# Optimization experiments

Hardware: AMD Instinct MI355X
Metric: run time of the kernel (lower is better)

## Reference

```python
import jax, jax.numpy as jnp
import numpy as np

# ---- config ----
N = 500000
C = 32            # output_coordinate_dim
RES = [256, 256, 256, 64]
J = 2             # wavelet levels
BOUNDS = 1.3
# plane i -> (H, W) of stored plane, and (q, r) coord indices into [x,y,z,t]
# grid_sample convention: coord0 indexes W, coord1 indexes H
PLANE_RES = [(256, 256), (256, 256), (256, 64), (256, 256), (256, 64), (256, 64)]
COORD_IDX = [(0, 1), (0, 2), (3, 0), (1, 2), (3, 1), (3, 2)]

# coif4 decomposition low-pass filter (pywt), 24 taps
DEC_LO = np.array([
    -1.7849850030882614e-06, -3.2596802368833675e-06, 3.1229875865345646e-05,
    6.233903446100713e-05, -0.00025997455248771324, -0.0005890207562443383,
    0.0012665619292989445, 0.003751436157278457, -0.00565828668661072,
    -0.015211731527946259, 0.025082261844864097, 0.03933442712333749,
    -0.09622044203398798, -0.06662747426342504, 0.4343860564914685,
    0.782238930920499, 0.41530840703043026, -0.05607731331675481,
    -0.08126669968087875, 0.026682300156053072, 0.016068943964776348,
    -0.0073461663276420935, -0.0016294920126017326, 0.0008923136685823146],
    dtype=np.float32)
REC_LO = DEC_LO[::-1].copy()                                    # synthesis low-pass
REC_HI = (DEC_LO * ((-1.0) ** np.arange(DEC_LO.shape[0]))).astype(np.float32)  # QMF high-pass


def _up2(x, axis):
    """Insert zeros between samples along axis (upsample by 2)."""
    x = jnp.moveaxis(x, axis, -1)
    z = jnp.zeros(x.shape[:-1] + (2 * x.shape[-1],), x.dtype)
    z = z.at[..., ::2].set(x)
    return jnp.moveaxis(z, -1, axis)


def _circ_conv(x, f, axis):
    """Circular convolution along axis with a short fixed filter (periodization mode)."""
    out = f[0] * x
    for k in range(1, len(f)):
        out = out + f[k] * jnp.roll(x, k, axis=axis)
    return out


def _sfb1d(lo, hi, axis):
    """1D synthesis filter bank: upsample, filter, add. Length L -> 2L."""
    return _circ_conv(_up2(lo, axis), REC_LO, axis) + _circ_conv(_up2(hi, axis), REC_HI, axis)


def _sfb_level(ll, yh):
    """One inverse-DWT level. ll: [1,C,h,w], yh: [1,C,3,h,w] -> [1,C,2h,2w]."""
    lh, hl, hh = yh[:, :, 0], yh[:, :, 1], yh[:, :, 2]
    lo = _sfb1d(ll, lh, axis=2)   # combine along H
    hi = _sfb1d(hl, hh, axis=2)
    return _sfb1d(lo, hi, axis=3)  # combine along W


def _idwt2(yl, yhb, yha):
    """2-level inverse DWT (coif4, periodization). yl coarsest, yhb coarse detail, yha fine detail."""
    x = _sfb_level(yl, yhb)   # H/4 -> H/2
    x = _sfb_level(x, yha)    # H/2 -> H
    return x                  # [1, C, H, W]


def _bilinear_sample(plane, coords):
    """torch.grid_sample(bilinear, align_corners=True) equivalent.
    plane: [C,H,W]; coords: [N,2] in [-1,1], coords[:,0]->W, coords[:,1]->H. Returns [N,C]."""
    Cc, H, W = plane.shape
    x = jnp.clip((coords[:, 0] + 1.0) * 0.5 * (W - 1), 0.0, W - 1.0)
    y = jnp.clip((coords[:, 1] + 1.0) * 0.5 * (H - 1), 0.0, H - 1.0)
    x0 = jnp.clip(jnp.floor(x), 0.0, W - 2.0)
    y0 = jnp.clip(jnp.floor(y), 0.0, H - 2.0)
    wx = x - x0
    wy = y - y0
    x0i = x0.astype(jnp.int32); x1i = x0i + 1
    y0i = y0.astype(jnp.int32); y1i = y0i + 1
    v = (plane[:, y0i, x0i] * (1 - wy) * (1 - wx)
         + plane[:, y0i, x1i] * (1 - wy) * wx
         + plane[:, y1i, x0i] * wy * (1 - wx)
         + plane[:, y1i, x1i] * wy * wx)  # [C,N]
    return v.T


def setup_inputs() -> dict:
    key = jax.random.key(0)
    keys = jax.random.split(key, 2 + 6 * 3)
    inp = {}
    inp["pts"] = jax.random.uniform(keys[0], (N, 3), jnp.float32, -BOUNDS, BOUNDS)
    inp["timestamps"] = jax.random.uniform(keys[1], (N, 1), jnp.float32, 0.0, 1.0)
    for i, (H, W) in enumerate(PLANE_RES):
        k0, k1, k2 = keys[2 + 3 * i], keys[2 + 3 * i + 1], keys[2 + 3 * i + 2]
        # wavelet-domain learned parameters: yl coarsest approx, yha fine detail, yhb coarse detail
        inp[f"yl{i}"] = 0.3 + 0.1 * jax.random.normal(k0, (1, C, H // 4, W // 4), jnp.float32)
        inp[f"yha{i}"] = 0.05 * jax.random.normal(k1, (1, C, 3, H // 2, W // 2), jnp.float32)
        inp[f"yhb{i}"] = 0.05 * jax.random.normal(k2, (1, C, 3, H // 4, W // 4), jnp.float32)
    return inp


def reference(pts, timestamps,
              yl0, yha0, yhb0, yl1, yha1, yhb1, yl2, yha2, yhb2,
              yl3, yha3, yhb3, yl4, yha4, yhb4, yl5, yha5, yhb5):
    coefs = [(yl0, yha0, yhb0), (yl1, yha1, yhb1), (yl2, yha2, yhb2),
             (yl3, yha3, yhb3), (yl4, yha4, yhb4), (yl5, yha5, yhb5)]
    # normalize_aabb with aabb = [[B,B,B],[-B,-B,-B]]
    pts_n = (pts - BOUNDS) * (2.0 / (-2.0 * BOUNDS)) - 1.0
    t = timestamps * 2.0 - 1.0
    p4 = jnp.concatenate([pts_n, t], axis=-1)  # [N,4] = (x,y,z,t) in [-1,1]
    interp = jnp.ones((), jnp.float32)
    for (yl, yha, yhb), (q, r) in zip(coefs, COORD_IDX):
        plane = _idwt2(yl, yhb, yha)[0]                      # [C,H,W] IDWT reconstruction
        coords = jnp.stack([p4[:, q], p4[:, r]], axis=-1)    # [N,2]
        feat = _bilinear_sample(plane, coords)               # [N,C] gather
        interp = interp * feat                               # multiplicative fusion
    return interp
```

## Files before the change

kernel.cpp:

```cpp
#include <hip/hip_runtime.h>
#include <hip/hip_fp16.h>

#define NBIN 4096
#define CAP 256
#define OVCAP 65536
#define NSB 32

__device__ __constant__ float DEC_LO[24] = {
    -1.7849850030882614e-06f, -3.2596802368833675e-06f, 3.1229875865345646e-05f,
    6.233903446100713e-05f, -0.00025997455248771324f, -0.0005890207562443383f,
    0.0012665619292989445f, 0.003751436157278457f, -0.00565828668661072f,
    -0.015211731527946259f, 0.025082261844864097f, 0.03933442712333749f,
    -0.09622044203398798f, -0.06662747426342504f, 0.4343860564914685f,
    0.782238930920499f, 0.41530840703043026f, -0.05607731331675481f,
    -0.08126669968087875f, 0.026682300156053072f, 0.016068943964776348f,
    -0.0073461663276420935f, -0.0016294920126017326f, 0.0008923136685823146f
};

struct PK {
    const float* yl[6];
    const float* yhb[6];
    const float* yha[6];
    float* x1[6];
    __half* lo2[6];
    __half* hi2[6];
    __half* planeH[6];
    const float* pts;
    const float* ts;
    int* cnt;
    float4* binP4;
    int* binIdx;
    float4* ovP4;
    int* ovIdx;
    int Npts;
};

__device__ __forceinline__ void compute_p4(const float* pts, const float* ts, int p, float* p4) {
    const float sc = (float)(2.0 / (-2.0 * 1.3));
    p4[0] = (pts[p * 3 + 0] - 1.3f) * sc - 1.0f;
    p4[1] = (pts[p * 3 + 1] - 1.3f) * sc - 1.0f;
    p4[2] = (pts[p * 3 + 2] - 1.3f) * sc - 1.0f;
    p4[3] = ts[p] * 2.0f - 1.0f;
}

__device__ __forceinline__ int morton_key(const float* p4) {
    int key = 0;
#pragma unroll
    for (int d = 0; d < 4; ++d) {
        float u = (p4[d] + 1.0f) * 0.5f * 8.0f;
        int ci = (int)u;
        ci = ci < 0 ? 0 : (ci > 7 ? 7 : ci);
#pragma unroll
        for (int b = 0; b < 3; ++b) key |= ((ci >> b) & 1) << (b * 4 + d);
    }
    return key;
}

__global__ __launch_bounds__(256) void k1_l1_zero(PK a) {
    __shared__ struct { float lo[32 * 64], hi[32 * 64]; } sm;
    int bid = blockIdx.x, tid = threadIdx.x;

    if (bid < 768) {
        int rg = bid & 3, c = (bid >> 2) & 31, i = bid >> 7;
        int w4 = (i == 0 || i == 1 || i == 3) ? 64 : 16;
        int lw4 = (w4 == 64) ? 6 : 4;

        const float* llc = a.yl[i] + (size_t)c * 64 * w4;
        const float* lhc = a.yhb[i] + (size_t)(c * 3 + 0) * 64 * w4;
        const float* hlc = a.yhb[i] + (size_t)(c * 3 + 1) * 64 * w4;
        const float* hhc = a.yhb[i] + (size_t)(c * 3 + 2) * 64 * w4;

        for (int idx = tid; idx < (16 << lw4); idx += 256) {
            int mp = idx >> lw4, x = idx & (w4 - 1);
            int m = rg * 16 + mp;
            float lo0 = 0.f, lo1 = 0.f, hi0 = 0.f, hi1 = 0.f;
#pragma unroll
            for (int j = 0; j < 12; ++j) {
                int r = (m - j) & 63;
                int ii = (r << lw4) + x;
                float vll = llc[ii], vlh = lhc[ii], vhl = hlc[ii], vhh = hhc[ii];
                float rl0 = DEC_LO[23 - 2 * j], rl1 = DEC_LO[22 - 2 * j];
                float rh0 = DEC_LO[2 * j],      rh1 = -DEC_LO[2 * j + 1];
                lo0 += rl0 * vll + rh0 * vlh;
                lo1 += rl1 * vll + rh1 * vlh;
                hi0 += rl0 * vhl + rh0 * vhh;
                hi1 += rl1 * vhl + rh1 * vhh;
            }
            sm.lo[((2 * mp) << lw4) + x] = lo0;
            sm.lo[((2 * mp + 1) << lw4) + x] = lo1;
            sm.hi[((2 * mp) << lw4) + x] = hi0;
            sm.hi[((2 * mp + 1) << lw4) + x] = hi1;
        }
        __syncthreads();

        int w2 = w4 * 2;
        float* x1p = a.x1[i] + (size_t)c * 128 * w2;
        for (int idx = tid; idx < (32 << lw4); idx += 256) {
            int yl = idx >> lw4, mcol = idx & (w4 - 1);
            float o0 = 0.f, o1 = 0.f;
#pragma unroll
            for (int j = 0; j < 12; ++j) {
                int r = (mcol - j) & (w4 - 1);
                float vl = sm.lo[(yl << lw4) + r], vh = sm.hi[(yl << lw4) + r];
                o0 += DEC_LO[23 - 2 * j] * vl + DEC_LO[2 * j] * vh;
                o1 += DEC_LO[22 - 2 * j] * vl - DEC_LO[2 * j + 1] * vh;
            }
            *(float2*)(x1p + (size_t)(rg * 32 + yl) * w2 + 2 * mcol) = make_float2(o0, o1);
        }
    } else {
        int idx = (bid - 768) * 256 + tid;
        if (idx <= NBIN) a.cnt[idx] = 0;
    }
}

__global__ __launch_bounds__(256) void k2_v2_scatter(PK a) {
    __shared__ int hist[NBIN];
    int bid = blockIdx.x, tid = threadIdx.x;

    if (bid < NSB) {
        for (int b = tid; b < NBIN; b += 256) hist[b] = 0;
        __syncthreads();

        int chunk = (a.Npts + NSB - 1) / NSB;
        int p0 = bid * chunk;
        int p1 = p0 + chunk; if (p1 > a.Npts) p1 = a.Npts;

        for (int p = p0 + tid; p < p1; p += 256) {
            float p4[4];
            compute_p4(a.pts, a.ts, p, p4);
            atomicAdd(&hist[morton_key(p4)], 1);
        }
        __syncthreads();

        for (int b = tid; b < NBIN; b += 256) {
            int h = hist[b];
            if (h > 0) hist[b] = atomicAdd(&a.cnt[b], h);
        }
        __syncthreads();

        for (int p = p0 + tid; p < p1; p += 256) {
            float p4[4];
            compute_p4(a.pts, a.ts, p, p4);
            int key = morton_key(p4);
            int pos = atomicAdd(&hist[key], 1);
            if (pos < CAP) {
                a.binP4[key * CAP + pos] = make_float4(p4[0], p4[1], p4[2], p4[3]);
                a.binIdx[key * CAP + pos] = p;
            } else {
                int ov = atomicAdd(&a.cnt[NBIN], 1);
                if (ov < OVCAP) {
                    a.ovP4[ov] = make_float4(p4[0], p4[1], p4[2], p4[3]);
                    a.ovIdx[ov] = p;
                }
            }
        }
    } else {
        int ib = bid - NSB;
        ib = (ib & 7) * 480 + (ib >> 3);

        const int boff[7] = {0, 1024, 2048, 2304, 3328, 3584, 3840};
        int i = 0;
        while (i < 5 && ib >= boff[i + 1]) ++i;
        int lw2 = (i == 0 || i == 1 || i == 3) ? 7 : 5;
        int w2 = 1 << lw2;
        unsigned t = (unsigned)(ib - boff[i]) * 256u + tid;
        unsigned hp = 128u << (lw2 - 1);
        unsigned c = t >> (6 + lw2);
        unsigned rem = t & (hp - 1);
        unsigned m = rem >> (lw2 - 1);
        unsigned x = (rem & (unsigned)((w2 >> 1) - 1)) * 2;
        unsigned hw = 128u << lw2;

        const float* llc = a.x1[i] + (size_t)c * hw;
        const float* lhc = a.yha[i] + (size_t)(c * 3 + 0) * hw;
        const float* hlc = a.yha[i] + (size_t)(c * 3 + 1) * hw;
        const float* hhc = a.yha[i] + (size_t)(c * 3 + 2) * hw;

        float lo0a = 0.f, lo0b = 0.f, lo1a = 0.f, lo1b = 0.f;
        float hi0a = 0.f, hi0b = 0.f, hi1a = 0.f, hi1b = 0.f;
#pragma unroll
        for (int j = 0; j < 12; ++j) {
            int r = ((int)m - j) & 127;
            unsigned idx = ((unsigned)r << lw2) + x;
            float2 vll = *(const float2*)(llc + idx);
            float2 vlh = *(const float2*)(lhc + idx);
            float2 vhl = *(const float2*)(hlc + idx);
            float2 vhh = *(const float2*)(hhc + idx);
            float rl0 = DEC_LO[23 - 2 * j], rl1 = DEC_LO[22 - 2 * j];
            float rh0 = DEC_LO[2 * j],      rh1 = -DEC_LO[2 * j + 1];
            lo0a += rl0 * vll.x + rh0 * vlh.x;  lo0b += rl0 * vll.y + rh0 * vlh.y;
            lo1a += rl1 * vll.x + rh1 * vlh.x;  lo1b += rl1 * vll.y + rh1 * vlh.y;
            hi0a += rl0 * vhl.x + rh0 * vhh.x;  hi0b += rl0 * vhl.y + rh0 * vhh.y;
            hi1a += rl1 * vhl.x + rh1 * vhh.x;  hi1b += rl1 * vhl.y + rh1 * vhh.y;
        }
        size_t ob = ((size_t)c * 256 + 2 * m) * w2 + x;
        *(__half2*)(a.lo2[i] + ob)      = __floats2half2_rn(lo0a, lo0b);
        *(__half2*)(a.lo2[i] + ob + w2) = __floats2half2_rn(lo1a, lo1b);
        *(__half2*)(a.hi2[i] + ob)      = __floats2half2_rn(hi0a, hi0b);
        *(__half2*)(a.hi2[i] + ob + w2) = __floats2half2_rn(hi1a, hi1b);
    }
}

__global__ __launch_bounds__(256) void k3_ht(PK a) {
    __shared__ struct { __half lo[32 * 130], hi[32 * 130]; } sm;
    int bid = blockIdx.x, tid = threadIdx.x;
    int i = bid >> 8, y = bid & 255;
    int lw2 = (i == 0 || i == 1 || i == 3) ? 7 : 5;
    int w2 = 1 << lw2;
    int stride = w2 + 2;

    for (int idx = tid; idx < (32 << lw2); idx += 256) {
        int c = idx >> lw2, x = idx & (w2 - 1);
        size_t g = ((size_t)c * 256 + y) * w2 + x;
        sm.lo[c * stride + x] = a.lo2[i][g];
        sm.hi[c * stride + x] = a.hi2[i][g];
    }
    __syncthreads();

    int W = 2 * w2;
    __half* orow = a.planeH[i] + (size_t)y * W * 32;
    for (int idx = tid; idx < (32 << lw2); idx += 256) {
        int m = idx >> 5, c = idx & 31;
        float o0 = 0.f, o1 = 0.f;
#pragma unroll
        for (int j = 0; j < 12; ++j) {
            int r2 = m - j; if (r2 < 0) r2 += w2;
            float vl = __half2float(sm.lo[c * stride + r2]);
            float vh = __half2float(sm.hi[c * stride + r2]);
            o0 += DEC_LO[23 - 2 * j] * vl + DEC_LO[2 * j] * vh;
            o1 += DEC_LO[22 - 2 * j] * vl - DEC_LO[2 * j + 1] * vh;
        }
        orow[(2 * m) * 32 + c] = __float2half(o0);
        orow[(2 * m + 1) * 32 + c] = __float2half(o1);
    }
}

union H8 { float4 f4; __half h[8]; };

struct SK {
    const __half* pl[6];
    const float4* binP4;
    const int* binIdx;
    const int* cnt;
    const float4* ovP4;
    const int* ovIdx;
    float* out;
};

__device__ __forceinline__ void sample_point(const SK& a, const float* p4, int oidx, int ch8) {
    const int PW[6] = {256, 256, 64, 256, 64, 64};
    const int QI[6] = {0, 0, 3, 1, 3, 3};
    const int RI[6] = {1, 2, 0, 2, 1, 2};
    float acc[8] = {1.f, 1.f, 1.f, 1.f, 1.f, 1.f, 1.f, 1.f};
#pragma unroll
    for (int i = 0; i < 6; ++i) {
        int W = PW[i];
        float cx = p4[QI[i]];
        float cy = p4[RI[i]];
        float fx = (cx + 1.0f) * 0.5f * (float)(W - 1);
        fx = fminf(fmaxf(fx, 0.0f), (float)(W - 1));
        float fy = (cy + 1.0f) * 0.5f * 255.0f;
        fy = fminf(fmaxf(fy, 0.0f), 255.0f);
        float x0 = fminf(fmaxf(floorf(fx), 0.0f), (float)(W - 2));
        float y0 = fminf(fmaxf(floorf(fy), 0.0f), 254.0f);
        float wx = fx - x0, wy = fy - y0;
        int xi = (int)x0, yi = (int)y0;

        const __half* base = a.pl[i] + ((size_t)yi * W + xi) * 32 + ch8;
        H8 u00, u01, u10, u11;
        u00.f4 = *(const float4*)(base);
        u01.f4 = *(const float4*)(base + 32);
        u10.f4 = *(const float4*)(base + (size_t)W * 32);
        u11.f4 = *(const float4*)(base + (size_t)W * 32 + 32);

        float w00 = (1.f - wy) * (1.f - wx), w01 = (1.f - wy) * wx;
        float w10 = wy * (1.f - wx), w11 = wy * wx;
#pragma unroll
        for (int k = 0; k < 8; ++k) {
            float f = w00 * __half2float(u00.h[k]) + w01 * __half2float(u01.h[k]) +
                      w10 * __half2float(u10.h[k]) + w11 * __half2float(u11.h[k]);
            acc[k] *= f;
        }
    }
    float* op = a.out + (size_t)oidx * 32 + ch8;
    *(float4*)(op) = make_float4(acc[0], acc[1], acc[2], acc[3]);
    *(float4*)(op + 4) = make_float4(acc[4], acc[5], acc[6], acc[7]);
}

__global__ __launch_bounds__(256) void k4_sample(SK a) {
    int bid = blockIdx.x, tid = threadIdx.x;
    if (bid < 2 * NBIN) {
        int b = bid & (NBIN - 1);
        int half = bid >> 12;
        int bin = (b & 7) * (NBIN / 8) + (b >> 3);
        int n = a.cnt[bin];
        n = n < CAP ? n : CAP;
        const float4* bp = a.binP4 + bin * CAP;
        const int* bi = a.binIdx + bin * CAP;
        for (int l = half * 256 + tid; l < n * 4; l += 512) {
            int s = l >> 2, ch8 = (l & 3) << 3;
            float4 q = bp[s];
            float p4[4] = {q.x, q.y, q.z, q.w};
            sample_point(a, p4, bi[s], ch8);
        }
    } else {
        int ov = a.cnt[NBIN];
        ov = ov < OVCAP ? ov : OVCAP;
        for (int l = (bid - 2 * NBIN) * 256 + tid; l < ov * 4; l += 8 * 256) {
            int s = l >> 2, ch8 = (l & 3) << 3;
            float4 q = a.ovP4[s];
            float p4[4] = {q.x, q.y, q.z, q.w};
            sample_point(a, p4, a.ovIdx[s], ch8);
        }
    }
}

extern "C" void kernel_launch(void* const* d_in, const int* in_sizes, int n_in,
                              void* d_out, int out_size, void* d_ws, size_t ws_size,
                              hipStream_t stream) {
    const int PWt[6] = {256, 256, 64, 256, 64, 64};
    const int Npts = in_sizes[0] / 3;

    char* ws = (char*)d_ws;
    PK a;
    size_t off = 0;
    for (int i = 0; i < 6; ++i) {
        int W = PWt[i], w2 = W / 2;
        a.x1[i] = (float*)(ws + off);      off += (size_t)32 * 128 * w2 * 4;
        a.lo2[i] = (__half*)(ws + off);    off += (size_t)32 * 256 * w2 * 2;
        a.hi2[i] = (__half*)(ws + off);    off += (size_t)32 * 256 * w2 * 2;
        a.planeH[i] = (__half*)(ws + off); off += (size_t)256 * W * 32 * 2;
    }
    off = (off + 15) & ~(size_t)15;
    a.binP4 = (float4*)(ws + off);  off += (size_t)NBIN * CAP * 16;
    a.ovP4 = (float4*)(ws + off);   off += (size_t)OVCAP * 16;
    a.binIdx = (int*)(ws + off);    off += (size_t)NBIN * CAP * 4;
    a.ovIdx = (int*)(ws + off);     off += (size_t)OVCAP * 4;
    a.cnt = (int*)(ws + off);       off += (NBIN + 1) * 4;

    a.pts = (const float*)d_in[0];
    a.ts = (const float*)d_in[1];
    for (int i = 0; i < 6; ++i) {
        a.yl[i] = (const float*)d_in[2 + 3 * i];
        a.yha[i] = (const float*)d_in[3 + 3 * i];
        a.yhb[i] = (const float*)d_in[4 + 3 * i];
    }
    a.Npts = Npts;

    k1_l1_zero<<<768 + 17, 256, 0, stream>>>(a);
    k2_v2_scatter<<<NSB + 3840, 256, 0, stream>>>(a);
    k3_ht<<<1536, 256, 0, stream>>>(a);

    SK s;
    for (int i = 0; i < 6; ++i) s.pl[i] = a.planeH[i];
    s.binP4 = a.binP4; s.binIdx = a.binIdx; s.cnt = a.cnt;
    s.ovP4 = a.ovP4; s.ovIdx = a.ovIdx;
    s.out = (float*)d_out;
    k4_sample<<<2 * NBIN + 8, 256, 0, stream>>>(s);
}
```

Before: 300.2 us.

## Replace block-local histogram scatter with replicated global-atomic bin counters

After: 263.4 us. -12.3%, faster.

```diff
diff --git a/kernel.cpp b/kernel.cpp
--- a/kernel.cpp
+++ b/kernel.cpp
@@ -2,9 +2,9 @@
 #include <hip/hip_fp16.h>
 
 #define NBIN 4096
-#define CAP 256
+#define NREP 8
+#define SCAP 32
 #define OVCAP 65536
-#define NSB 32
 
 __device__ __constant__ float DEC_LO[24] = {
     -1.7849850030882614e-06f, -3.2596802368833675e-06f, 3.1229875865345646e-05f,
@@ -109,53 +109,54 @@
         }
     } else {
         int idx = (bid - 768) * 256 + tid;
-        if (idx <= NBIN) a.cnt[idx] = 0;
+        if (idx <= NREP * NBIN) a.cnt[idx] = 0;
     }
 }
 
 __global__ __launch_bounds__(256) void k2_v2_scatter(PK a) {
-    __shared__ int hist[NBIN];
     int bid = blockIdx.x, tid = threadIdx.x;
 
-    if (bid < NSB) {
-        for (int b = tid; b < NBIN; b += 256) hist[b] = 0;
-        __syncthreads();
-
-        int chunk = (a.Npts + NSB - 1) / NSB;
-        int p0 = bid * chunk;
-        int p1 = p0 + chunk; if (p1 > a.Npts) p1 = a.Npts;
-
-        for (int p = p0 + tid; p < p1; p += 256) {
-            float p4[4];
-            compute_p4(a.pts, a.ts, p, p4);
-            atomicAdd(&hist[morton_key(p4)], 1);
-        }
-        __syncthreads();
-
-        for (int b = tid; b < NBIN; b += 256) {
-            int h = hist[b];
-            if (h > 0) hist[b] = atomicAdd(&a.cnt[b], h);
-        }
-        __syncthreads();
-
-        for (int p = p0 + tid; p < p1; p += 256) {
-            float p4[4];
-            compute_p4(a.pts, a.ts, p, p4);
-            int key = morton_key(p4);
-            int pos = atomicAdd(&hist[key], 1);
-            if (pos < CAP) {
-                a.binP4[key * CAP + pos] = make_float4(p4[0], p4[1], p4[2], p4[3]);
-                a.binIdx[key * CAP + pos] = p;
-            } else {
-                int ov = atomicAdd(&a.cnt[NBIN], 1);
-                if (ov < OVCAP) {
-                    a.ovP4[ov] = make_float4(p4[0], p4[1], p4[2], p4[3]);
-                    a.ovIdx[ov] = p;
+    if (bid < 512) {
+        const int S = 512 * 256;
+        int rep = bid & 7;
+        int t = bid * 256 + tid;
+        for (int base = 0; base < a.Npts; base += 4 * S) {
+            float4 q[4];
+            int key[4], pi[4], pos[4];
+#pragma unroll
+            for (int k = 0; k < 4; ++k) {
+                int p = base + t + k * S;
+                pi[k] = p;
+                if (p < a.Npts) {
+                    float p4[4];
+                    compute_p4(a.pts, a.ts, p, p4);
+                    key[k] = morton_key(p4);
+                    q[k] = make_float4(p4[0], p4[1], p4[2], p4[3]);
+                } else {
+                    key[k] = -1;
                 }
             }
+#pragma unroll
+            for (int k = 0; k < 4; ++k)
+                if (key[k] >= 0) pos[k] = atomicAdd(&a.cnt[rep * NBIN + key[k]], 1);
+#pragma unroll
+            for (int k = 0; k < 4; ++k) {
+                if (key[k] < 0) continue;
+                if (pos[k] < SCAP) {
+                    size_t slot = ((size_t)rep * NBIN + key[k]) * SCAP + pos[k];
+                    a.binP4[slot] = q[k];
+                    a.binIdx[slot] = pi[k];
+                } else {
+                    int ov = atomicAdd(&a.cnt[NREP * NBIN], 1);
+                    if (ov < OVCAP) {
+                        a.ovP4[ov] = q[k];
+                        a.ovIdx[ov] = pi[k];
+                    }
+                }
+            }
         }
     } else {
-        int ib = bid - NSB;
+        int ib = bid - 512;
         ib = (ib & 7) * 480 + (ib >> 3);
 
         const int boff[7] = {0, 1024, 2048, 2304, 3328, 3584, 3840};
@@ -293,18 +294,28 @@
         int b = bid & (NBIN - 1);
         int half = bid >> 12;
         int bin = (b & 7) * (NBIN / 8) + (b >> 3);
-        int n = a.cnt[bin];
-        n = n < CAP ? n : CAP;
-        const float4* bp = a.binP4 + bin * CAP;
-        const int* bi = a.binIdx + bin * CAP;
-        for (int l = half * 256 + tid; l < n * 4; l += 512) {
+
+        int pre[NREP + 1];
+        pre[0] = 0;
+#pragma unroll
+        for (int r = 0; r < NREP; ++r) {
+            int c = a.cnt[r * NBIN + bin];
+            pre[r + 1] = pre[r] + (c < SCAP ? c : SCAP);
+        }
+        int total = pre[NREP];
+
+        for (int l = half * 256 + tid; l < total * 4; l += 512) {
             int s = l >> 2, ch8 = (l & 3) << 3;
-            float4 q = bp[s];
+            int r = 0;
+#pragma unroll
+            for (int rr = 1; rr < NREP; ++rr) if (s >= pre[rr]) r = rr;
+            size_t slot = ((size_t)r * NBIN + bin) * SCAP + (s - pre[r]);
+            float4 q = a.binP4[slot];
             float p4[4] = {q.x, q.y, q.z, q.w};
-            sample_point(a, p4, bi[s], ch8);
+            sample_point(a, p4, a.binIdx[slot], ch8);
         }
     } else {
-        int ov = a.cnt[NBIN];
+        int ov = a.cnt[NREP * NBIN];
         ov = ov < OVCAP ? ov : OVCAP;
         for (int l = (bid - 2 * NBIN) * 256 + tid; l < ov * 4; l += 8 * 256) {
             int s = l >> 2, ch8 = (l & 3) << 3;
@@ -332,11 +343,11 @@
         a.planeH[i] = (__half*)(ws + off); off += (size_t)256 * W * 32 * 2;
     }
     off = (off + 15) & ~(size_t)15;
-    a.binP4 = (float4*)(ws + off);  off += (size_t)NBIN * CAP * 16;
+    a.binP4 = (float4*)(ws + off);  off += (size_t)NREP * NBIN * SCAP * 16;
     a.ovP4 = (float4*)(ws + off);   off += (size_t)OVCAP * 16;
-    a.binIdx = (int*)(ws + off);    off += (size_t)NBIN * CAP * 4;
+    a.binIdx = (int*)(ws + off);    off += (size_t)NREP * NBIN * SCAP * 4;
     a.ovIdx = (int*)(ws + off);     off += (size_t)OVCAP * 4;
-    a.cnt = (int*)(ws + off);       off += (NBIN + 1) * 4;
+    a.cnt = (int*)(ws + off);       off += ((size_t)NREP * NBIN + 1) * 4;
 
     a.pts = (const float*)d_in[0];
     a.ts = (const float*)d_in[1];
@@ -347,8 +358,8 @@
     }
     a.Npts = Npts;
 
-    k1_l1_zero<<<768 + 17, 256, 0, stream>>>(a);
-    k2_v2_scatter<<<NSB + 3840, 256, 0, stream>>>(a);
+    k1_l1_zero<<<768 + 129, 256, 0, stream>>>(a);
+    k2_v2_scatter<<<512 + 3840, 256, 0, stream>>>(a);
     k3_ht<<<1536, 256, 0, stream>>>(a);
 
     SK s;
```
